# Performance work log

Measured on AMD Instinct MI355X. Metric: run time of the kernel, lower is better.

Reference implementation:

```python
import jax, jax.numpy as jnp
import numpy as np

B, N, DIM = 4, 16384, 512
H, D, S = 8, 64, 64  # heads, dim_head, n_global_queries
SCALE = 1.0  # FLARE hardcodes scale=1.0


def setup_inputs() -> dict:
    key = jax.random.key(0)
    ks = jax.random.split(key, 10)
    inner = H * D
    s = 0.02
    return {
        "x": jax.random.normal(ks[0], (B, N, DIM), dtype=jnp.float32),
        "q_global": jax.random.normal(ks[1], (1, H, S, D), dtype=jnp.float32),
        "Wx": jax.random.normal(ks[2], (DIM, inner), dtype=jnp.float32) * s,
        "bx": jnp.zeros((inner,), dtype=jnp.float32),
        "Wk": jax.random.normal(ks[3], (D, D), dtype=jnp.float32) * s,
        "bk": jnp.zeros((D,), dtype=jnp.float32),
        "Wv": jax.random.normal(ks[4], (D, D), dtype=jnp.float32) * s,
        "bv": jnp.zeros((D,), dtype=jnp.float32),
        "Wo": jax.random.normal(ks[5], (inner, DIM), dtype=jnp.float32) * s,
        "bo": jnp.zeros((DIM,), dtype=jnp.float32),
    }


def reference(x, q_global, Wx, bx, Wk, bk, Wv, bv, Wo, bo):
    b, n, c = x.shape
    # input projection + split heads: B N (H D) -> B H N D
    x_mid = (x @ Wx + bx).reshape(b, n, H, D).transpose(0, 2, 1, 3)
    # per-head k/v projections (dim_head x dim_head)
    k = x_mid @ Wk + bk  # [B,H,N,D]
    v = x_mid @ Wv + bv  # [B,H,N,D]
    G = q_global  # broadcast over batch
    # pass 1: aggregate tokens into S global slots
    attn1 = jax.nn.softmax(jnp.einsum('bhsd,bhnd->bhsn', jnp.broadcast_to(G, (b, H, S, D)), k) * SCALE, axis=-1)
    z = jnp.einsum('bhsn,bhnd->bhsd', attn1, v)  # [B,H,S,D]
    # pass 2: distribute slots back to tokens (query=k, key=G, value=z)
    attn2 = jax.nn.softmax(jnp.einsum('bhnd,bhsd->bhns', k, jnp.broadcast_to(G, (b, H, S, D))) * SCALE, axis=-1)
    y = jnp.einsum('bhns,bhsd->bhnd', attn2, z)  # [B,H,N,D]
    # merge heads + output projection
    out = y.transpose(0, 2, 1, 3).reshape(b, n, H * D)
    return out @ Wo + bo
```

## Files before the change

kernel.cpp:

```cpp
#include <hip/hip_runtime.h>
#include <stdint.h>

#define DEV __device__ __forceinline__

typedef __attribute__((ext_vector_type(8))) short bf16x8;
typedef __attribute__((ext_vector_type(4))) float f32x4;
typedef __attribute__((ext_vector_type(8))) unsigned short u16x8;

DEV unsigned short f2bf(float f) {
  union { float f; unsigned int u; } v; v.f = f;
  unsigned int u = v.u;
  return (unsigned short)((u + 0x7FFFu + ((u >> 16) & 1u)) >> 16);
}
DEV float bf2f(unsigned short u) {
  union { unsigned int u; float f; } v; v.u = ((unsigned int)u) << 16;
  return v.f;
}
DEV f32x4 mfma16(bf16x8 a, bf16x8 b, f32x4 c) {
  return __builtin_amdgcn_mfma_f32_16x16x32_bf16(a, b, c, 0, 0, 0);
}
DEV void gl_lds16(const void* g, void* l) {
  __builtin_amdgcn_global_load_lds(
      (const __attribute__((address_space(1))) void*)g,
      (__attribute__((address_space(3))) void*)l, 16, 0, 0);
}

__global__ __launch_bounds__(256) void k_cvt_bf16(const float* __restrict__ in,
                                                  unsigned short* __restrict__ out,
                                                  int n8) {
  int i = blockIdx.x * 256 + threadIdx.x;
  if (i >= n8) return;
  const float4* p = (const float4*)in + (size_t)i * 2;
  float4 a = p[0], b = p[1];
  u16x8 o;
  o[0] = f2bf(a.x); o[1] = f2bf(a.y); o[2] = f2bf(a.z); o[3] = f2bf(a.w);
  o[4] = f2bf(b.x); o[5] = f2bf(b.y); o[6] = f2bf(b.z); o[7] = f2bf(b.w);
  ((u16x8*)out)[i] = o;
}

__global__ void k_gk(const float* __restrict__ Wk, const float* __restrict__ qg,
                     float* __restrict__ GK) {
  int idx = blockIdx.x * 256 + threadIdx.x;
  int dd = idx & 63, hs = idx >> 6;
  float a = 0.f;
#pragma unroll 8
  for (int d = 0; d < 64; ++d) a += Wk[dd * 64 + d] * qg[(size_t)hs * 64 + d];
  GK[idx] = a;
}

__global__ void k_wl(const float* __restrict__ Wx, const float* __restrict__ GK,
                     unsigned short* __restrict__ Wcat) {
  int idx = blockIdx.x * 256 + threadIdx.x;
  int c = idx & 511, hs = idx >> 9;
  int h = hs >> 6, s = hs & 63;
  float a = 0.f;
#pragma unroll 8
  for (int dd = 0; dd < 64; ++dd) a += Wx[(size_t)c * 512 + h * 64 + dd] * GK[hs * 64 + dd];
  Wcat[(size_t)(h * 128 + s) * 512 + c] = f2bf(a);
}

__global__ void k_wv(const float* __restrict__ Wx, const float* __restrict__ Wv,
                     unsigned short* __restrict__ Wcat) {
  int idx = blockIdx.x * 256 + threadIdx.x;
  int c = idx & 511, o = idx >> 9;
  int h = o >> 6, dp = o & 63;
  float a = 0.f;
#pragma unroll 8
  for (int dd = 0; dd < 64; ++dd) a += Wx[(size_t)c * 512 + h * 64 + dd] * Wv[dd * 64 + dp];
  Wcat[(size_t)(h * 128 + 64 + dp) * 512 + c] = f2bf(a);
}

__global__ void k_bias2(const float* __restrict__ bx, const float* __restrict__ bk,
                        const float* __restrict__ bv, const float* __restrict__ Wv,
                        const float* __restrict__ qg, const float* __restrict__ GK,
                        float* __restrict__ bias) {
  int o = blockIdx.x * 256 + threadIdx.x;
  if (o >= 1024) return;
  int h = o >> 7, j = o & 127;
  if (j < 64) {
    int hs = h * 64 + j;
    float a = 0.f;
    for (int dd = 0; dd < 64; ++dd) a += bx[h * 64 + dd] * GK[(size_t)hs * 64 + dd];
    for (int dp = 0; dp < 64; ++dp) a += bk[dp] * qg[(size_t)hs * 64 + dp];
    bias[o] = a;
  } else {
    int dp = j - 64;
    float a = bv[dp];
    for (int dd = 0; dd < 64; ++dd) a += bx[h * 64 + dd] * Wv[dd * 64 + dp];
    bias[o] = a;
  }
}

__global__ void k_wo_t(const float* __restrict__ Wo, unsigned short* __restrict__ WoT) {
  int idx = blockIdx.x * 256 + threadIdx.x;
  int i = idx >> 9, o = idx & 511;
  WoT[(size_t)o * 512 + i] = f2bf(Wo[(size_t)i * 512 + o]);
}

template <int MODE>
__global__ __launch_bounds__(256, 4) void k_mm(const unsigned short* __restrict__ A,
                                               const unsigned short* __restrict__ BTg,
                                               const float* __restrict__ bias,
                                               unsigned short* __restrict__ P2,
                                               float* __restrict__ zpart,
                                               float* __restrict__ dpart,
                                               float* __restrict__ outF) {
  __shared__ __align__(16) char lds[35328];
  const int tid = threadIdx.x;
  const int w = tid >> 6, lane = tid & 63, l = lane & 15, g = lane >> 4;
  unsigned bid = blockIdx.x;
  int mtile, ntile;
  if (MODE == 1) {
    unsigned nbid = (bid & 7) * 512 + (bid >> 3);
    mtile = nbid >> 3;
    ntile = nbid & 7;
  } else {
    unsigned nbid = (bid & 7) * 256 + (bid >> 3);
    mtile = nbid >> 2;
    ntile = nbid & 3;
  }
  const int bm = mtile * 128;
  const int bn = ntile * 128;
  const int b = mtile >> 7;
  const unsigned short* BT = (MODE == 0) ? BTg + ((size_t)b << 18) : BTg;
  const int wm = (w >> 1) * 64, wn = (w & 1) * 64;
  char* As = lds;
  char* Bs = lds + 16384;
  f32x4 acc[4][4] = {};
  const int sw = (l & 7) << 4;

  for (int t = 0; t < 8; ++t) {
#pragma unroll
    for (int i = 0; i < 4; ++i) {
      int off = i * 4096 + tid * 16;
      int row = off >> 7;
      int cb = (off & 127) ^ ((row & 7) << 4);
      gl_lds16(A + (size_t)(bm + row) * 512 + t * 64 + (cb >> 1), As + off);
      gl_lds16(BT + (size_t)(bn + row) * 512 + t * 64 + (cb >> 1), Bs + off);
    }
    __syncthreads();
#pragma unroll
    for (int ks = 0; ks < 2; ++ks) {
      int kb = (ks * 64 + g * 16) ^ sw;
      bf16x8 af[4], bf[4];
#pragma unroll
      for (int fm = 0; fm < 4; ++fm)
        af[fm] = *(const bf16x8*)(As + (wm + fm * 16 + l) * 128 + kb);
#pragma unroll
      for (int fn = 0; fn < 4; ++fn)
        bf[fn] = *(const bf16x8*)(Bs + (wn + fn * 16 + l) * 128 + kb);
#pragma unroll
      for (int fm = 0; fm < 4; ++fm)
#pragma unroll
        for (int fn = 0; fn < 4; ++fn)
          acc[fm][fn] = mfma16(af[fm], bf[fn], acc[fm][fn]);
    }
    __syncthreads();
  }

  if (MODE == 0) {
#pragma unroll
    for (int fm = 0; fm < 4; ++fm)
#pragma unroll
      for (int fn = 0; fn < 4; ++fn) {
        int col = bn + wn + fn * 16 + l;
        float bb = bias[col];
#pragma unroll
        for (int r = 0; r < 4; ++r)
          outF[(size_t)(bm + wm + fm * 16 + g * 4 + r) * 512 + col] = acc[fm][fn][r] + bb;
      }
    return;
  }

  const int h = ntile;
  unsigned short* ET = (unsigned short*)lds;
  unsigned short* VT = (unsigned short*)(lds + 17408);
  float* denp = (float*)(lds + 34816);
  float bc[4];
#pragma unroll
  for (int fn = 0; fn < 4; ++fn) bc[fn] = bias[h * 128 + wn + fn * 16 + l];
  if (wn == 0) {
#pragma unroll
    for (int fm = 0; fm < 4; ++fm)
#pragma unroll
      for (int fn = 0; fn < 4; ++fn)
#pragma unroll
        for (int r = 0; r < 4; ++r)
          acc[fm][fn][r] = __expf(acc[fm][fn][r] + bc[fn] - 8.0f);
#pragma unroll
    for (int fm = 0; fm < 4; ++fm) {
      f32x4 rs;
#pragma unroll
      for (int r = 0; r < 4; ++r) {
        float t2 = (acc[fm][0][r] + acc[fm][1][r]) + (acc[fm][2][r] + acc[fm][3][r]);
#pragma unroll
        for (int m = 1; m < 16; m <<= 1) t2 += __shfl_xor(t2, m);
        rs[r] = t2;
      }
#pragma unroll
      for (int r = 0; r < 4; ++r) {
        float rinv = 1.f / rs[r];
        int n = bm + wm + fm * 16 + g * 4 + r;
#pragma unroll
        for (int fn = 0; fn < 4; ++fn)
          P2[(size_t)n * 512 + h * 64 + fn * 16 + l] = f2bf(acc[fm][fn][r] * rinv);
      }
    }
#pragma unroll
    for (int fm = 0; fm < 4; ++fm)
#pragma unroll
      for (int fn = 0; fn < 4; ++fn)
#pragma unroll
        for (int r = 0; r < 4; ++r)
          ET[(fn * 16 + l) * 136 + wm + fm * 16 + g * 4 + r] = f2bf(acc[fm][fn][r]);
#pragma unroll
    for (int fn = 0; fn < 4; ++fn) {
      float t2 = 0.f;
#pragma unroll
      for (int fm = 0; fm < 4; ++fm)
#pragma unroll
        for (int r = 0; r < 4; ++r) t2 += acc[fm][fn][r];
      t2 += __shfl_xor(t2, 16);
      t2 += __shfl_xor(t2, 32);
      if (g == 0) denp[(w >> 1) * 64 + fn * 16 + l] = t2;
    }
  } else {
#pragma unroll
    for (int fm = 0; fm < 4; ++fm)
#pragma unroll
      for (int fn = 0; fn < 4; ++fn)
#pragma unroll
        for (int r = 0; r < 4; ++r)
          VT[(fn * 16 + l) * 136 + wm + fm * 16 + g * 4 + r] =
              f2bf(acc[fm][fn][r] + bc[fn]);
  }
  __syncthreads();
  f32x4 za[4] = {};
#pragma unroll
  for (int ks2 = 0; ks2 < 4; ++ks2) {
    bf16x8 a2 = *(const bf16x8*)&ET[(w * 16 + l) * 136 + ks2 * 32 + g * 8];
#pragma unroll
    for (int fd = 0; fd < 4; ++fd) {
      bf16x8 b2 = *(const bf16x8*)&VT[(fd * 16 + l) * 136 + ks2 * 32 + g * 8];
      za[fd] = mfma16(a2, b2, za[fd]);
    }
  }
  size_t mh = (size_t)mtile * 8 + h;
#pragma unroll
  for (int fd = 0; fd < 4; ++fd)
#pragma unroll
    for (int r = 0; r < 4; ++r)
      zpart[mh * 4096 + (w * 16 + g * 4 + r) * 64 + fd * 16 + l] = za[fd][r];
  if (w == 0) dpart[mh * 64 + lane] = denp[lane] + denp[64 + lane];
}

__global__ void k_zred(const float* __restrict__ zpart, const float* __restrict__ dpart,
                       float* __restrict__ z) {
  int idx = blockIdx.x * 256 + threadIdx.x;
  int bh = idx >> 12, s = (idx >> 6) & 63, d = idx & 63;
  int b = bh >> 3, h = bh & 7;
  float num = 0.f, den = 0.f;
  for (int mm = 0; mm < 128; ++mm) {
    size_t mh = ((size_t)(b * 128 + mm)) * 8 + h;
    num += zpart[mh * 4096 + s * 64 + d];
    den += dpart[mh * 64 + s];
  }
  z[idx] = num / den;
}

__global__ void k_zwo(const float* __restrict__ z, const unsigned short* __restrict__ WoT,
                      unsigned short* __restrict__ zWoT) {
  int idx = blockIdx.x * 256 + threadIdx.x;
  int hs = idx & 511, c = (idx >> 9) & 511, b = idx >> 18;
  int h = hs >> 6;
  const float* zp = z + ((size_t)(b * 8 + h) * 64 + (hs & 63)) * 64;
  const unsigned short* wp = WoT + (size_t)c * 512 + h * 64;
  float a = 0.f;
#pragma unroll 8
  for (int d = 0; d < 64; ++d) a += zp[d] * bf2f(wp[d]);
  zWoT[((size_t)(b * 512) + c) * 512 + hs] = f2bf(a);
}

extern "C" void kernel_launch(void* const* d_in, const int* in_sizes, int n_in,
                              void* d_out, int out_size, void* d_ws, size_t ws_size,
                              hipStream_t stream) {
  const float* x  = (const float*)d_in[0];
  const float* qg = (const float*)d_in[1];
  const float* Wx = (const float*)d_in[2];
  const float* bx = (const float*)d_in[3];
  const float* Wk = (const float*)d_in[4];
  const float* bk = (const float*)d_in[5];
  const float* Wv = (const float*)d_in[6];
  const float* bv = (const float*)d_in[7];
  const float* Wo = (const float*)d_in[8];
  const float* bo = (const float*)d_in[9];
  float* out = (float*)d_out;

  char* ws = (char*)d_ws;
  unsigned short* xbf  = (unsigned short*)(ws);
  unsigned short* P2   = (unsigned short*)(ws + 67108864);
  unsigned short* Wcat = (unsigned short*)(ws + 134217728);
  unsigned short* WoT  = (unsigned short*)(ws + 135266304);
  float* bias          = (float*)(ws + 135790592);
  float* GK            = (float*)(ws + 135794688);
  unsigned short* zWoT = (unsigned short*)(ws + 135925760);
  float* zbuf          = (float*)(ws + 138027008);
  char* dob = (char*)d_out;
  float* zpart = (float*)(dob);
  float* dpart = (float*)(dob + 67108864);

  k_cvt_bf16<<<dim3(16384), dim3(256), 0, stream>>>(x, xbf, 4194304);
  k_gk<<<dim3(128), dim3(256), 0, stream>>>(Wk, qg, GK);
  k_wl<<<dim3(1024), dim3(256), 0, stream>>>(Wx, GK, Wcat);
  k_wv<<<dim3(1024), dim3(256), 0, stream>>>(Wx, Wv, Wcat);
  k_bias2<<<dim3(4), dim3(256), 0, stream>>>(bx, bk, bv, Wv, qg, GK, bias);
  k_wo_t<<<dim3(1024), dim3(256), 0, stream>>>(Wo, WoT);
  k_mm<1><<<dim3(4096), dim3(256), 0, stream>>>(xbf, Wcat, bias, P2, zpart, dpart, nullptr);
  k_zred<<<dim3(512), dim3(256), 0, stream>>>(zpart, dpart, zbuf);
  k_zwo<<<dim3(4096), dim3(256), 0, stream>>>(zbuf, WoT, zWoT);
  k_mm<0><<<dim3(2048), dim3(256), 0, stream>>>(P2, zWoT, bo, nullptr, nullptr, nullptr, out);
}
```

Baseline: 284.1 us.

## Merge setup kernels and accumulate four M-tiles per block in pass-1 GEMM

```diff
diff --git a/kernel.cpp b/kernel.cpp
--- a/kernel.cpp
+++ b/kernel.cpp
@@ -25,76 +25,79 @@
       (__attribute__((address_space(3))) void*)l, 16, 0, 0);
 }
 
-__global__ __launch_bounds__(256) void k_cvt_bf16(const float* __restrict__ in,
-                                                  unsigned short* __restrict__ out,
-                                                  int n8) {
-  int i = blockIdx.x * 256 + threadIdx.x;
-  if (i >= n8) return;
-  const float4* p = (const float4*)in + (size_t)i * 2;
-  float4 a = p[0], b = p[1];
-  u16x8 o;
-  o[0] = f2bf(a.x); o[1] = f2bf(a.y); o[2] = f2bf(a.z); o[3] = f2bf(a.w);
-  o[4] = f2bf(b.x); o[5] = f2bf(b.y); o[6] = f2bf(b.z); o[7] = f2bf(b.w);
-  ((u16x8*)out)[i] = o;
-}
-
-__global__ void k_gk(const float* __restrict__ Wk, const float* __restrict__ qg,
-                     float* __restrict__ GK) {
-  int idx = blockIdx.x * 256 + threadIdx.x;
-  int dd = idx & 63, hs = idx >> 6;
-  float a = 0.f;
+__global__ __launch_bounds__(256) void k_misc1(const float* __restrict__ x,
+                                               unsigned short* __restrict__ xbf,
+                                               const float* __restrict__ Wk,
+                                               const float* __restrict__ qg,
+                                               float* __restrict__ GK) {
+  int bid = blockIdx.x;
+  if (bid < 16384) {
+    int i = bid * 256 + threadIdx.x;
+    const float4* p = (const float4*)x + (size_t)i * 2;
+    float4 a = p[0], b = p[1];
+    u16x8 o;
+    o[0] = f2bf(a.x); o[1] = f2bf(a.y); o[2] = f2bf(a.z); o[3] = f2bf(a.w);
+    o[4] = f2bf(b.x); o[5] = f2bf(b.y); o[6] = f2bf(b.z); o[7] = f2bf(b.w);
+    ((u16x8*)xbf)[i] = o;
+  } else {
+    int idx = (bid - 16384) * 256 + threadIdx.x;
+    int dd = idx & 63, hs = idx >> 6;
+    float a = 0.f;
 #pragma unroll 8
-  for (int d = 0; d < 64; ++d) a += Wk[dd * 64 + d] * qg[(size_t)hs * 64 + d];
-  GK[idx] = a;
-}
-
-__global__ void k_wl(const float* __restrict__ Wx, const float* __restrict__ GK,
-                     unsigned short* __restrict__ Wcat) {
-  int idx = blockIdx.x * 256 + threadIdx.x;
-  int c = idx & 511, hs = idx >> 9;
-  int h = hs >> 6, s = hs & 63;
-  float a = 0.f;
+    for (int d = 0; d < 64; ++d) a += Wk[dd * 64 + d] * qg[(size_t)hs * 64 + d];
+    GK[idx] = a;
+  }
+}
+
+__global__ __launch_bounds__(256) void k_misc2(const float* __restrict__ Wx,
+                                               const float* __restrict__ Wv,
+                                               const float* __restrict__ Wo,
+                                               const float* __restrict__ bx,
+                                               const float* __restrict__ bk,
+                                               const float* __restrict__ bv,
+                                               const float* __restrict__ qg,
+                                               const float* __restrict__ GK,
+                                               unsigned short* __restrict__ Wcat,
+                                               unsigned short* __restrict__ WoT,
+                                               float* __restrict__ bias) {
+  int bid = blockIdx.x;
+  if (bid < 1024) {
+    int idx = bid * 256 + threadIdx.x;
+    int c = idx & 511, hs = idx >> 9;
+    int h = hs >> 6, s = hs & 63;
+    float a = 0.f;
 #pragma unroll 8
-  for (int dd = 0; dd < 64; ++dd) a += Wx[(size_t)c * 512 + h * 64 + dd] * GK[hs * 64 + dd];
-  Wcat[(size_t)(h * 128 + s) * 512 + c] = f2bf(a);
-}
-
-__global__ void k_wv(const float* __restrict__ Wx, const float* __restrict__ Wv,
-                     unsigned short* __restrict__ Wcat) {
-  int idx = blockIdx.x * 256 + threadIdx.x;
-  int c = idx & 511, o = idx >> 9;
-  int h = o >> 6, dp = o & 63;
-  float a = 0.f;
+    for (int dd = 0; dd < 64; ++dd) a += Wx[(size_t)c * 512 + h * 64 + dd] * GK[hs * 64 + dd];
+    Wcat[(size_t)(h * 128 + s) * 512 + c] = f2bf(a);
+  } else if (bid < 2048) {
+    int idx = (bid - 1024) * 256 + threadIdx.x;
+    int c = idx & 511, o = idx >> 9;
+    int h = o >> 6, dp = o & 63;
+    float a = 0.f;
 #pragma unroll 8
-  for (int dd = 0; dd < 64; ++dd) a += Wx[(size_t)c * 512 + h * 64 + dd] * Wv[dd * 64 + dp];
-  Wcat[(size_t)(h * 128 + 64 + dp) * 512 + c] = f2bf(a);
-}
-
-__global__ void k_bias2(const float* __restrict__ bx, const float* __restrict__ bk,
-                        const float* __restrict__ bv, const float* __restrict__ Wv,
-                        const float* __restrict__ qg, const float* __restrict__ GK,
-                        float* __restrict__ bias) {
-  int o = blockIdx.x * 256 + threadIdx.x;
-  if (o >= 1024) return;
-  int h = o >> 7, j = o & 127;
-  if (j < 64) {
-    int hs = h * 64 + j;
-    float a = 0.f;
-    for (int dd = 0; dd < 64; ++dd) a += bx[h * 64 + dd] * GK[(size_t)hs * 64 + dd];
-    for (int dp = 0; dp < 64; ++dp) a += bk[dp] * qg[(size_t)hs * 64 + dp];
-    bias[o] = a;
+    for (int dd = 0; dd < 64; ++dd) a += Wx[(size_t)c * 512 + h * 64 + dd] * Wv[dd * 64 + dp];
+    Wcat[(size_t)(h * 128 + 64 + dp) * 512 + c] = f2bf(a);
+  } else if (bid < 3072) {
+    int idx = (bid - 2048) * 256 + threadIdx.x;
+    int i = idx >> 9, o = idx & 511;
+    WoT[(size_t)o * 512 + i] = f2bf(Wo[(size_t)i * 512 + o]);
   } else {
-    int dp = j - 64;
-    float a = bv[dp];
-    for (int dd = 0; dd < 64; ++dd) a += bx[h * 64 + dd] * Wv[dd * 64 + dp];
-    bias[o] = a;
-  }
-}
-
-__global__ void k_wo_t(const float* __restrict__ Wo, unsigned short* __restrict__ WoT) {
-  int idx = blockIdx.x * 256 + threadIdx.x;
-  int i = idx >> 9, o = idx & 511;
-  WoT[(size_t)o * 512 + i] = f2bf(Wo[(size_t)i * 512 + o]);
+    int o = (bid - 3072) * 256 + threadIdx.x;
+    if (o >= 1024) return;
+    int h = o >> 7, j = o & 127;
+    if (j < 64) {
+      int hs = h * 64 + j;
+      float a = 0.f;
+      for (int dd = 0; dd < 64; ++dd) a += bx[h * 64 + dd] * GK[(size_t)hs * 64 + dd];
+      for (int dp = 0; dp < 64; ++dp) a += bk[dp] * qg[(size_t)hs * 64 + dp];
+      bias[o] = a;
+    } else {
+      int dp = j - 64;
+      float a = bv[dp];
+      for (int dd = 0; dd < 64; ++dd) a += bx[h * 64 + dd] * Wv[dd * 64 + dp];
+      bias[o] = a;
+    }
+  }
 }
 
 template <int MODE>
@@ -109,149 +112,160 @@
   const int tid = threadIdx.x;
   const int w = tid >> 6, lane = tid & 63, l = lane & 15, g = lane >> 4;
   unsigned bid = blockIdx.x;
-  int mtile, ntile;
+  int group = 0, h = 0, mtile = 0, ntile = 0;
   if (MODE == 1) {
-    unsigned nbid = (bid & 7) * 512 + (bid >> 3);
-    mtile = nbid >> 3;
-    ntile = nbid & 7;
+    unsigned nbid = (bid & 7) * 128 + (bid >> 3);
+    group = nbid >> 3;
+    h = nbid & 7;
+    ntile = h;
   } else {
     unsigned nbid = (bid & 7) * 256 + (bid >> 3);
     mtile = nbid >> 2;
     ntile = nbid & 3;
   }
-  const int bm = mtile * 128;
   const int bn = ntile * 128;
-  const int b = mtile >> 7;
-  const unsigned short* BT = (MODE == 0) ? BTg + ((size_t)b << 18) : BTg;
   const int wm = (w >> 1) * 64, wn = (w & 1) * 64;
   char* As = lds;
   char* Bs = lds + 16384;
-  f32x4 acc[4][4] = {};
-  const int sw = (l & 7) << 4;
-
-  for (int t = 0; t < 8; ++t) {
-#pragma unroll
-    for (int i = 0; i < 4; ++i) {
-      int off = i * 4096 + tid * 16;
-      int row = off >> 7;
-      int cb = (off & 127) ^ ((row & 7) << 4);
-      gl_lds16(A + (size_t)(bm + row) * 512 + t * 64 + (cb >> 1), As + off);
-      gl_lds16(BT + (size_t)(bn + row) * 512 + t * 64 + (cb >> 1), Bs + off);
-    }
-    __syncthreads();
-#pragma unroll
-    for (int ks = 0; ks < 2; ++ks) {
-      int kb = (ks * 64 + g * 16) ^ sw;
-      bf16x8 af[4], bf[4];
-#pragma unroll
-      for (int fm = 0; fm < 4; ++fm)
-        af[fm] = *(const bf16x8*)(As + (wm + fm * 16 + l) * 128 + kb);
-#pragma unroll
-      for (int fn = 0; fn < 4; ++fn)
-        bf[fn] = *(const bf16x8*)(Bs + (wn + fn * 16 + l) * 128 + kb);
-#pragma unroll
-      for (int fm = 0; fm < 4; ++fm)
-#pragma unroll
-        for (int fn = 0; fn < 4; ++fn)
-          acc[fm][fn] = mfma16(af[fm], bf[fn], acc[fm][fn]);
-    }
-    __syncthreads();
-  }
-
-  if (MODE == 0) {
-#pragma unroll
-    for (int fm = 0; fm < 4; ++fm)
-#pragma unroll
-      for (int fn = 0; fn < 4; ++fn) {
-        int col = bn + wn + fn * 16 + l;
-        float bb = bias[col];
-#pragma unroll
-        for (int r = 0; r < 4; ++r)
-          outF[(size_t)(bm + wm + fm * 16 + g * 4 + r) * 512 + col] = acc[fm][fn][r] + bb;
-      }
-    return;
-  }
-
-  const int h = ntile;
   unsigned short* ET = (unsigned short*)lds;
   unsigned short* VT = (unsigned short*)(lds + 17408);
   float* denp = (float*)(lds + 34816);
-  float bc[4];
-#pragma unroll
-  for (int fn = 0; fn < 4; ++fn) bc[fn] = bias[h * 128 + wn + fn * 16 + l];
-  if (wn == 0) {
-#pragma unroll
-    for (int fm = 0; fm < 4; ++fm)
-#pragma unroll
-      for (int fn = 0; fn < 4; ++fn)
-#pragma unroll
-        for (int r = 0; r < 4; ++r)
-          acc[fm][fn][r] = __expf(acc[fm][fn][r] + bc[fn] - 8.0f);
-#pragma unroll
-    for (int fm = 0; fm < 4; ++fm) {
-      f32x4 rs;
-#pragma unroll
-      for (int r = 0; r < 4; ++r) {
-        float t2 = (acc[fm][0][r] + acc[fm][1][r]) + (acc[fm][2][r] + acc[fm][3][r]);
-#pragma unroll
-        for (int m = 1; m < 16; m <<= 1) t2 += __shfl_xor(t2, m);
-        rs[r] = t2;
-      }
-#pragma unroll
-      for (int r = 0; r < 4; ++r) {
-        float rinv = 1.f / rs[r];
-        int n = bm + wm + fm * 16 + g * 4 + r;
+  const int sw = (l & 7) << 4;
+  f32x4 za[4] = {};
+  float dtot = 0.f;
+
+  for (int mt = 0; mt < (MODE ? 4 : 1); ++mt) {
+    const int bm = MODE ? (group * 4 + mt) * 128 : mtile * 128;
+    const unsigned short* BT = (MODE == 0) ? BTg + ((size_t)(bm >> 14) << 18) : BTg;
+    f32x4 acc[4][4] = {};
+    for (int t = 0; t < 8; ++t) {
+#pragma unroll
+      for (int i = 0; i < 4; ++i) {
+        int off = i * 4096 + tid * 16;
+        int row = off >> 7;
+        int cb = (off & 127) ^ ((row & 7) << 4);
+        gl_lds16(A + (size_t)(bm + row) * 512 + t * 64 + (cb >> 1), As + off);
+        gl_lds16(BT + (size_t)(bn + row) * 512 + t * 64 + (cb >> 1), Bs + off);
+      }
+      __syncthreads();
+#pragma unroll
+      for (int ks = 0; ks < 2; ++ks) {
+        int kb = (ks * 64 + g * 16) ^ sw;
+        bf16x8 af[4], bf[4];
+#pragma unroll
+        for (int fm = 0; fm < 4; ++fm)
+          af[fm] = *(const bf16x8*)(As + (wm + fm * 16 + l) * 128 + kb);
 #pragma unroll
         for (int fn = 0; fn < 4; ++fn)
-          P2[(size_t)n * 512 + h * 64 + fn * 16 + l] = f2bf(acc[fm][fn][r] * rinv);
-      }
-    }
-#pragma unroll
-    for (int fm = 0; fm < 4; ++fm)
-#pragma unroll
-      for (int fn = 0; fn < 4; ++fn)
-#pragma unroll
-        for (int r = 0; r < 4; ++r)
-          ET[(fn * 16 + l) * 136 + wm + fm * 16 + g * 4 + r] = f2bf(acc[fm][fn][r]);
-#pragma unroll
-    for (int fn = 0; fn < 4; ++fn) {
-      float t2 = 0.f;
+          bf[fn] = *(const bf16x8*)(Bs + (wn + fn * 16 + l) * 128 + kb);
+#pragma unroll
+        for (int fm = 0; fm < 4; ++fm)
+#pragma unroll
+          for (int fn = 0; fn < 4; ++fn)
+            acc[fm][fn] = (MODE == 0) ? mfma16(bf[fn], af[fm], acc[fm][fn])
+                                      : mfma16(af[fm], bf[fn], acc[fm][fn]);
+      }
+      __syncthreads();
+    }
+
+    if (MODE == 0) {
+#pragma unroll
+      for (int fm = 0; fm < 4; ++fm) {
+        int row = bm + wm + fm * 16 + l;
+#pragma unroll
+        for (int fn = 0; fn < 4; ++fn) {
+          int col0 = bn + wn + fn * 16 + g * 4;
+          f32x4 b4 = *(const f32x4*)&bias[col0];
+          f32x4 o;
+#pragma unroll
+          for (int r = 0; r < 4; ++r) o[r] = acc[fm][fn][r] + b4[r];
+          *(f32x4*)&outF[(size_t)row * 512 + col0] = o;
+        }
+      }
+      return;
+    }
+
+    float bc[4];
+#pragma unroll
+    for (int fn = 0; fn < 4; ++fn) bc[fn] = bias[h * 128 + wn + fn * 16 + l];
+    if (wn == 0) {
 #pragma unroll
       for (int fm = 0; fm < 4; ++fm)
 #pragma unroll
-        for (int r = 0; r < 4; ++r) t2 += acc[fm][fn][r];
-      t2 += __shfl_xor(t2, 16);
-      t2 += __shfl_xor(t2, 32);
-      if (g == 0) denp[(w >> 1) * 64 + fn * 16 + l] = t2;
-    }
-  } else {
-#pragma unroll
-    for (int fm = 0; fm < 4; ++fm)
-#pragma unroll
-      for (int fn = 0; fn < 4; ++fn)
-#pragma unroll
-        for (int r = 0; r < 4; ++r)
-          VT[(fn * 16 + l) * 136 + wm + fm * 16 + g * 4 + r] =
-              f2bf(acc[fm][fn][r] + bc[fn]);
-  }
-  __syncthreads();
-  f32x4 za[4] = {};
-#pragma unroll
-  for (int ks2 = 0; ks2 < 4; ++ks2) {
-    bf16x8 a2 = *(const bf16x8*)&ET[(w * 16 + l) * 136 + ks2 * 32 + g * 8];
-#pragma unroll
-    for (int fd = 0; fd < 4; ++fd) {
-      bf16x8 b2 = *(const bf16x8*)&VT[(fd * 16 + l) * 136 + ks2 * 32 + g * 8];
-      za[fd] = mfma16(a2, b2, za[fd]);
-    }
-  }
-  size_t mh = (size_t)mtile * 8 + h;
-#pragma unroll
-  for (int fd = 0; fd < 4; ++fd)
-#pragma unroll
-    for (int r = 0; r < 4; ++r)
-      zpart[mh * 4096 + (w * 16 + g * 4 + r) * 64 + fd * 16 + l] = za[fd][r];
-  if (w == 0) dpart[mh * 64 + lane] = denp[lane] + denp[64 + lane];
+        for (int fn = 0; fn < 4; ++fn)
+#pragma unroll
+          for (int r = 0; r < 4; ++r)
+            acc[fm][fn][r] = __expf(acc[fm][fn][r] + bc[fn] - 8.0f);
+#pragma unroll
+      for (int fm = 0; fm < 4; ++fm) {
+        f32x4 rs;
+#pragma unroll
+        for (int r = 0; r < 4; ++r) {
+          float t2 = (acc[fm][0][r] + acc[fm][1][r]) + (acc[fm][2][r] + acc[fm][3][r]);
+#pragma unroll
+          for (int m = 1; m < 16; m <<= 1) t2 += __shfl_xor(t2, m);
+          rs[r] = t2;
+        }
+#pragma unroll
+        for (int r = 0; r < 4; ++r) {
+          float rinv = 1.f / rs[r];
+          int n = bm + wm + fm * 16 + g * 4 + r;
+#pragma unroll
+          for (int fn = 0; fn < 4; ++fn)
+            P2[(size_t)n * 512 + h * 64 + fn * 16 + l] = f2bf(acc[fm][fn][r] * rinv);
+        }
+      }
+#pragma unroll
+      for (int fm = 0; fm < 4; ++fm)
+#pragma unroll
+        for (int fn = 0; fn < 4; ++fn)
+#pragma unroll
+          for (int r = 0; r < 4; ++r)
+            ET[(fn * 16 + l) * 136 + wm + fm * 16 + g * 4 + r] = f2bf(acc[fm][fn][r]);
+#pragma unroll
+      for (int fn = 0; fn < 4; ++fn) {
+        float t2 = 0.f;
+#pragma unroll
+        for (int fm = 0; fm < 4; ++fm)
+#pragma unroll
+          for (int r = 0; r < 4; ++r) t2 += acc[fm][fn][r];
+        t2 += __shfl_xor(t2, 16);
+        t2 += __shfl_xor(t2, 32);
+        if (g == 0) denp[(w >> 1) * 64 + fn * 16 + l] = t2;
+      }
+    } else {
+#pragma unroll
+      for (int fm = 0; fm < 4; ++fm)
+#pragma unroll
+        for (int fn = 0; fn < 4; ++fn)
+#pragma unroll
+          for (int r = 0; r < 4; ++r)
+            VT[(fn * 16 + l) * 136 + wm + fm * 16 + g * 4 + r] =
+                f2bf(acc[fm][fn][r] + bc[fn]);
+    }
+    __syncthreads();
+#pragma unroll
+    for (int ks2 = 0; ks2 < 4; ++ks2) {
+      bf16x8 a2 = *(const bf16x8*)&ET[(w * 16 + l) * 136 + ks2 * 32 + g * 8];
+#pragma unroll
+      for (int fd = 0; fd < 4; ++fd) {
+        bf16x8 b2 = *(const bf16x8*)&VT[(fd * 16 + l) * 136 + ks2 * 32 + g * 8];
+        za[fd] = mfma16(a2, b2, za[fd]);
+      }
+    }
+    dtot += denp[lane] + denp[64 + lane];
+    __syncthreads();
+  }
+
+  if (MODE == 1) {
+    size_t mh = (size_t)group * 8 + h;
+#pragma unroll
+    for (int fd = 0; fd < 4; ++fd)
+#pragma unroll
+      for (int r = 0; r < 4; ++r)
+        zpart[mh * 4096 + (w * 16 + g * 4 + r) * 64 + fd * 16 + l] = za[fd][r];
+    if (w == 0) dpart[mh * 64 + lane] = dtot;
+  }
 }
 
 __global__ void k_zred(const float* __restrict__ zpart, const float* __restrict__ dpart,
@@ -260,8 +274,8 @@
   int bh = idx >> 12, s = (idx >> 6) & 63, d = idx & 63;
   int b = bh >> 3, h = bh & 7;
   float num = 0.f, den = 0.f;
-  for (int mm = 0; mm < 128; ++mm) {
-    size_t mh = ((size_t)(b * 128 + mm)) * 8 + h;
+  for (int c = 0; c < 32; ++c) {
+    size_t mh = ((size_t)(b * 32 + c)) * 8 + h;
     num += zpart[mh * 4096 + s * 64 + d];
     den += dpart[mh * 64 + s];
   }
@@ -307,15 +321,12 @@
   float* zbuf          = (float*)(ws + 138027008);
   char* dob = (char*)d_out;
   float* zpart = (float*)(dob);
-  float* dpart = (float*)(dob + 67108864);
-
-  k_cvt_bf16<<<dim3(16384), dim3(256), 0, stream>>>(x, xbf, 4194304);
-  k_gk<<<dim3(128), dim3(256), 0, stream>>>(Wk, qg, GK);
-  k_wl<<<dim3(1024), dim3(256), 0, stream>>>(Wx, GK, Wcat);
-  k_wv<<<dim3(1024), dim3(256), 0, stream>>>(Wx, Wv, Wcat);
-  k_bias2<<<dim3(4), dim3(256), 0, stream>>>(bx, bk, bv, Wv, qg, GK, bias);
-  k_wo_t<<<dim3(1024), dim3(256), 0, stream>>>(Wo, WoT);
-  k_mm<1><<<dim3(4096), dim3(256), 0, stream>>>(xbf, Wcat, bias, P2, zpart, dpart, nullptr);
+  float* dpart = (float*)(dob + 16777216);
+
+  k_misc1<<<dim3(16512), dim3(256), 0, stream>>>(x, xbf, Wk, qg, GK);
+  k_misc2<<<dim3(3076), dim3(256), 0, stream>>>(Wx, Wv, Wo, bx, bk, bv, qg, GK,
+                                                Wcat, WoT, bias);
+  k_mm<1><<<dim3(1024), dim3(256), 0, stream>>>(xbf, Wcat, bias, P2, zpart, dpart, nullptr);
   k_zred<<<dim3(512), dim3(256), 0, stream>>>(zpart, dpart, zbuf);
   k_zwo<<<dim3(4096), dim3(256), 0, stream>>>(zbuf, WoT, zWoT);
   k_mm<0><<<dim3(2048), dim3(256), 0, stream>>>(P2, zWoT, bo, nullptr, nullptr, nullptr, out);
```

After: 402.5 us. 41.7% more time.
